# Performance work log

Hardware: AMD Instinct MI355X
Metric: run time of the kernel (lower is better)

The kernel has to match this reference:

```python
import jax, jax.numpy as jnp
import numpy as np

V, D, NL, NC = 16, 256, 4, 2
MAXL, NSTATE, DCONV, EXPAND, HEADDIM = 1024, 64, 4, 2, 64
DIN = EXPAND * D            # 512 inner channels
H = DIN // HEADDIM          # 8 heads
P = HEADDIM                 # 64 head dim
CONV_DIM = DIN + 2 * NSTATE # 640 channels through depthwise conv
D_IN_PROJ = 2 * DIN + 2 * NSTATE + H  # 1160
B_, L_ = 2, 1024
EPS = 1e-5


def setup_inputs() -> dict:
    key = jax.random.key(0)
    ks = iter(jax.random.split(key, 32))

    def rn(shape, s=0.02):
        return jax.random.normal(next(ks), shape, jnp.float32) * s

    emb = rn((V, D)).at[4].set(0.0)  # padding_idx=4 row zeroed
    pos_emb = rn((MAXL, D))
    in_proj_w = rn((NL, D_IN_PROJ, D))
    conv_w = rn((NL, CONV_DIM, DCONV), 0.1)
    conv_b = rn((NL, CONV_DIM), 0.1)
    dt_bias = rn((NL, H), 0.5)
    A_log = jnp.log(jax.random.uniform(next(ks), (NL, H), jnp.float32, 1.0, 16.0))
    D_param = jnp.ones((NL, H), jnp.float32)
    norm_w = jnp.ones((NL, DIN), jnp.float32)
    out_proj_w = rn((NL, D, DIN))
    pooler_w = rn((D, D), 0.05)
    pooler_b = jnp.zeros((D,), jnp.float32)
    cls1_w = rn((D // 2, D), 0.05)
    cls1_b = jnp.zeros((D // 2,), jnp.float32)
    cls2_w = rn((NC, D // 2), 0.05)
    cls2_b = jnp.zeros((NC,), jnp.float32)
    input_ids = jax.random.randint(next(ks), (B_, L_), 0, V)
    return dict(input_ids=input_ids, emb=emb, pos_emb=pos_emb,
                in_proj_w=in_proj_w, conv_w=conv_w, conv_b=conv_b,
                dt_bias=dt_bias, A_log=A_log, D_param=D_param, norm_w=norm_w,
                out_proj_w=out_proj_w, pooler_w=pooler_w, pooler_b=pooler_b,
                cls1_w=cls1_w, cls1_b=cls1_b, cls2_w=cls2_w, cls2_b=cls2_b)


def _mamba2(x, Win, cw, cb, dtb, A_log, Dp, nw, Wout):
    Bsz, L, _ = x.shape
    zxbcdt = jnp.einsum('bld,pd->blp', x, Win)              # (B,L,2*DIN+2N+H)
    z = zxbcdt[..., :DIN]
    xBC = zxbcdt[..., DIN:DIN + CONV_DIM]
    dt = jax.nn.softplus(zxbcdt[..., -H:] + dtb)            # (B,L,H)
    # causal depthwise conv over time
    xBC = jnp.transpose(xBC, (0, 2, 1))                     # (B,C,L)
    xBC = jax.lax.conv_general_dilated(
        xBC, cw[:, None, :], (1,), [(DCONV - 1, 0)],
        dimension_numbers=('NCH', 'OIH', 'NCH'),
        feature_group_count=CONV_DIM)
    xBC = jax.nn.silu(jnp.transpose(xBC, (0, 2, 1)) + cb)   # (B,L,C)
    xs = xBC[..., :DIN].reshape(Bsz, L, H, P)
    Bm = xBC[..., DIN:DIN + NSTATE]                         # (B,L,N)
    Cm = xBC[..., DIN + NSTATE:]                            # (B,L,N)
    A = -jnp.exp(A_log)                                     # (H,)
    dA = jnp.exp(dt * A)                                    # (B,L,H)
    dBx = dt[..., None, None] * xs[..., None] * Bm[:, :, None, None, :]  # (B,L,H,P,N)

    def step(h, inp):
        dA_t, dBx_t, C_t = inp
        h = dA_t[:, :, None, None] * h + dBx_t              # (B,H,P,N)
        y = jnp.einsum('bhpn,bn->bhp', h, C_t)
        return h, y

    h0 = jnp.zeros((Bsz, H, P, NSTATE), x.dtype)
    _, y = jax.lax.scan(step, h0, (jnp.moveaxis(dA, 1, 0),
                                   jnp.moveaxis(dBx, 1, 0),
                                   jnp.moveaxis(Cm, 1, 0)))
    y = jnp.moveaxis(y, 0, 1) + Dp[None, None, :, None] * xs  # (B,L,H,P)
    y = y.reshape(Bsz, L, DIN) * jax.nn.silu(z)               # gated
    y = y * jax.lax.rsqrt(jnp.mean(y * y, axis=-1, keepdims=True) + EPS) * nw
    return jnp.einsum('bld,od->blo', y, Wout)


def reference(input_ids, emb, pos_emb, in_proj_w, conv_w, conv_b, dt_bias,
              A_log, D_param, norm_w, out_proj_w, pooler_w, pooler_b,
              cls1_w, cls1_b, cls2_w, cls2_b):
    L = input_ids.shape[1]
    x = emb[input_ids] + pos_emb[:L][None]                  # (B,L,D)
    for i in range(NL):
        x = x + _mamba2(x, in_proj_w[i], conv_w[i], conv_b[i], dt_bias[i],
                        A_log[i], D_param[i], norm_w[i], out_proj_w[i])
    pooled = (x.mean(axis=1) + x.max(axis=1)) * 0.5         # (B,D)
    pooled = jax.nn.gelu(pooled @ pooler_w.T + pooler_b, approximate=False)
    hcls = jax.nn.gelu(pooled @ cls1_w.T + cls1_b, approximate=False)
    return hcls @ cls2_w.T + cls2_b
```

## Files before the change

### kernel.cpp

```cpp
#include <hip/hip_runtime.h>
#include <math.h>

#define D_ 256
#define NL_ 4
#define NC_ 2
#define L_LEN 1024
#define NSTATE_ 64
#define DIN_ 512
#define H_ 8
#define P_ 64
#define CONVDIM_ 640
#define DPROJ_ 1160
#define EPS_ 1e-5f
#define NCH_ 16

typedef __attribute__((ext_vector_type(8))) short short8;
typedef __attribute__((ext_vector_type(4))) float f32x4;
typedef __attribute__((ext_vector_type(4))) unsigned short us4;

__device__ __forceinline__ float siluf(float x) { return x / (1.f + __expf(-x)); }
__device__ __forceinline__ float geluf(float x) { return 0.5f * x * (1.f + erff(x * 0.70710678118654752f)); }
__device__ __forceinline__ unsigned short f2bf(float f) {
    unsigned u = __float_as_uint(f);
    u += 0x7FFFu + ((u >> 16) & 1u);
    return (unsigned short)(u >> 16);
}
__device__ __forceinline__ float bf2f(unsigned short h) {
    return __uint_as_float(((unsigned)h) << 16);
}

__global__ void k_embed(const int* __restrict__ ids, const float* __restrict__ emb,
                        const float* __restrict__ pos, float* __restrict__ x, int total) {
    int i = blockIdx.x * blockDim.x + threadIdx.x;
    if (i >= total) return;
    int d = i & (D_ - 1);
    int bl = i >> 8;
    int l = bl & (L_LEN - 1);
    x[i] = emb[ids[bl] * D_ + d] + pos[l * D_ + d];
}

__global__ void k_w2bf2(const float* __restrict__ Wi, const float* __restrict__ Wo,
                        unsigned short* __restrict__ wih, unsigned short* __restrict__ wil,
                        unsigned short* __restrict__ woh, unsigned short* __restrict__ wol,
                        int nin, int ntot) {
    int i = blockIdx.x * blockDim.x + threadIdx.x;
    if (i >= ntot) return;
    if (i < nin) {
        float f = Wi[i];
        unsigned short h = f2bf(f);
        wih[i] = h;
        wil[i] = f2bf(f - bf2f(h));
    } else {
        int j = i - nin;
        float f = Wo[j];
        unsigned short h = f2bf(f);
        woh[j] = h;
        wol[j] = f2bf(f - bf2f(h));
    }
}

__global__ void __launch_bounds__(256) gemm_bf3(const float* __restrict__ A,
        const unsigned short* __restrict__ Bhi, const unsigned short* __restrict__ Blo,
        float* __restrict__ C, int M, int N, int K, int kchunk) {
    __shared__ __align__(16) unsigned short Ah[128 * 40];
    __shared__ __align__(16) unsigned short Al[128 * 40];
    __shared__ __align__(16) unsigned short Bh[64 * 40];
    __shared__ __align__(16) unsigned short Bl[64 * 40];
    const int tid = threadIdx.x;
    const int col0 = blockIdx.x * 64;
    const int row0 = blockIdx.y * 128;
    const int kbase = blockIdx.z * kchunk;

    const int sar = tid >> 1, sas = (tid & 1) * 16;
    const int sbr = tid >> 2, sbs = (tid & 3) * 8;
    const bool bok = (col0 + sbr) < N;
    const float* aptr = A + (size_t)(row0 + sar) * K + kbase + sas;
    const unsigned short* bhptr = Bhi + (size_t)(col0 + sbr) * K + kbase + sbs;
    const unsigned short* blptr = Blo + (size_t)(col0 + sbr) * K + kbase + sbs;

    float4 pa[4];
    short8 pbh = {0, 0, 0, 0, 0, 0, 0, 0}, pbl = {0, 0, 0, 0, 0, 0, 0, 0};
#pragma unroll
    for (int i = 0; i < 4; ++i) pa[i] = *(const float4*)(aptr + i * 4);
    if (bok) {
        pbh = *(const short8*)bhptr;
        pbl = *(const short8*)blptr;
    }

    const int wave = tid >> 6, lane = tid & 63;
    const int lq = lane >> 4, lm = lane & 15;
    f32x4 acc[2][4] = {};
    const int nsteps = kchunk >> 5;
    for (int s = 0; s < nsteps; ++s) {
        __syncthreads();
#pragma unroll
        for (int i = 0; i < 4; ++i) {
            float4 f = pa[i];
            unsigned short h0 = f2bf(f.x), h1 = f2bf(f.y), h2 = f2bf(f.z), h3 = f2bf(f.w);
            us4 hv = {h0, h1, h2, h3};
            us4 lv = {f2bf(f.x - bf2f(h0)), f2bf(f.y - bf2f(h1)),
                      f2bf(f.z - bf2f(h2)), f2bf(f.w - bf2f(h3))};
            *(us4*)&Ah[sar * 40 + sas + i * 4] = hv;
            *(us4*)&Al[sar * 40 + sas + i * 4] = lv;
        }
        *(short8*)&Bh[sbr * 40 + sbs] = pbh;
        *(short8*)&Bl[sbr * 40 + sbs] = pbl;
        __syncthreads();
        if (s + 1 < nsteps) {
            int ko = (s + 1) * 32;
#pragma unroll
            for (int i = 0; i < 4; ++i) pa[i] = *(const float4*)(aptr + ko + i * 4);
            if (bok) {
                pbh = *(const short8*)(bhptr + ko);
                pbl = *(const short8*)(blptr + ko);
            }
        }
        short8 bh[4], bl[4];
#pragma unroll
        for (int ct = 0; ct < 4; ++ct) {
            bh[ct] = *(const short8*)&Bh[(ct * 16 + lm) * 40 + lq * 8];
            bl[ct] = *(const short8*)&Bl[(ct * 16 + lm) * 40 + lq * 8];
        }
#pragma unroll
        for (int rt = 0; rt < 2; ++rt) {
            short8 ah = *(const short8*)&Ah[(wave * 32 + rt * 16 + lm) * 40 + lq * 8];
            short8 al = *(const short8*)&Al[(wave * 32 + rt * 16 + lm) * 40 + lq * 8];
#pragma unroll
            for (int ct = 0; ct < 4; ++ct) {
                acc[rt][ct] = __builtin_amdgcn_mfma_f32_16x16x32_bf16(ah, bh[ct], acc[rt][ct], 0, 0, 0);
                acc[rt][ct] = __builtin_amdgcn_mfma_f32_16x16x32_bf16(ah, bl[ct], acc[rt][ct], 0, 0, 0);
                acc[rt][ct] = __builtin_amdgcn_mfma_f32_16x16x32_bf16(al, bh[ct], acc[rt][ct], 0, 0, 0);
            }
        }
    }
#pragma unroll
    for (int rt = 0; rt < 2; ++rt) {
#pragma unroll
        for (int ct = 0; ct < 4; ++ct) {
            int col = col0 + ct * 16 + lm;
            if (col >= N) continue;
            int rbase = row0 + wave * 32 + rt * 16 + lq * 4;
#pragma unroll
            for (int reg = 0; reg < 4; ++reg) {
                size_t idx = (size_t)(rbase + reg) * N + col;
                C[idx] = acc[rt][ct][reg];
            }
        }
    }
}

__global__ void __launch_bounds__(256) gemm_outs(const float* __restrict__ y,
        const float* __restrict__ nw, const float* __restrict__ rowssq,
        const unsigned short* __restrict__ Bhi, const unsigned short* __restrict__ Blo,
        float* __restrict__ x) {
    __shared__ __align__(16) unsigned short Ah[128 * 40];
    __shared__ __align__(16) unsigned short Al[128 * 40];
    __shared__ __align__(16) unsigned short Bh[64 * 40];
    __shared__ __align__(16) unsigned short Bl[64 * 40];
    const int tid = threadIdx.x;
    const int col0 = blockIdx.x * 64;
    const int row0 = blockIdx.y * 128;
    const int kbase = blockIdx.z * 128;
    const int sar = tid >> 1, sas = (tid & 1) * 16;
    const int sbr = tid >> 2, sbs = (tid & 3) * 8;
    const float* yp = y + (size_t)(row0 + sar) * DIN_ + kbase + sas;
    const unsigned short* bhptr = Bhi + (size_t)(col0 + sbr) * DIN_ + kbase + sbs;
    const unsigned short* blptr = Blo + (size_t)(col0 + sbr) * DIN_ + kbase + sbs;
    const float sc = rsqrtf(rowssq[row0 + sar] * (1.f / DIN_) + EPS_);

    float4 py[4], pnw[4];
    short8 pbh, pbl;
#pragma unroll
    for (int i = 0; i < 4; ++i) {
        py[i] = *(const float4*)(yp + i * 4);
        pnw[i] = *(const float4*)&nw[kbase + sas + i * 4];
    }
    pbh = *(const short8*)bhptr;
    pbl = *(const short8*)blptr;

    const int wave = tid >> 6, lane = tid & 63;
    const int lq = lane >> 4, lm = lane & 15;
    f32x4 acc[2][4] = {};
    for (int s = 0; s < 4; ++s) {
        __syncthreads();
#pragma unroll
        for (int i = 0; i < 4; ++i) {
            float4 fy = py[i], fn = pnw[i];
            float g0 = fy.x * sc * fn.x;
            float g1 = fy.y * sc * fn.y;
            float g2 = fy.z * sc * fn.z;
            float g3 = fy.w * sc * fn.w;
            unsigned short h0 = f2bf(g0), h1 = f2bf(g1), h2 = f2bf(g2), h3 = f2bf(g3);
            us4 hv = {h0, h1, h2, h3};
            us4 lv = {f2bf(g0 - bf2f(h0)), f2bf(g1 - bf2f(h1)),
                      f2bf(g2 - bf2f(h2)), f2bf(g3 - bf2f(h3))};
            *(us4*)&Ah[sar * 40 + sas + i * 4] = hv;
            *(us4*)&Al[sar * 40 + sas + i * 4] = lv;
        }
        *(short8*)&Bh[sbr * 40 + sbs] = pbh;
        *(short8*)&Bl[sbr * 40 + sbs] = pbl;
        __syncthreads();
        if (s + 1 < 4) {
            int ko = (s + 1) * 32;
#pragma unroll
            for (int i = 0; i < 4; ++i) {
                py[i] = *(const float4*)(yp + ko + i * 4);
                pnw[i] = *(const float4*)&nw[kbase + ko + sas + i * 4];
            }
            pbh = *(const short8*)(bhptr + ko);
            pbl = *(const short8*)(blptr + ko);
        }
        short8 bh[4], bl[4];
#pragma unroll
        for (int ct = 0; ct < 4; ++ct) {
            bh[ct] = *(const short8*)&Bh[(ct * 16 + lm) * 40 + lq * 8];
            bl[ct] = *(const short8*)&Bl[(ct * 16 + lm) * 40 + lq * 8];
        }
#pragma unroll
        for (int rt = 0; rt < 2; ++rt) {
            short8 ah = *(const short8*)&Ah[(wave * 32 + rt * 16 + lm) * 40 + lq * 8];
            short8 al = *(const short8*)&Al[(wave * 32 + rt * 16 + lm) * 40 + lq * 8];
#pragma unroll
            for (int ct = 0; ct < 4; ++ct) {
                acc[rt][ct] = __builtin_amdgcn_mfma_f32_16x16x32_bf16(ah, bh[ct], acc[rt][ct], 0, 0, 0);
                acc[rt][ct] = __builtin_amdgcn_mfma_f32_16x16x32_bf16(ah, bl[ct], acc[rt][ct], 0, 0, 0);
                acc[rt][ct] = __builtin_amdgcn_mfma_f32_16x16x32_bf16(al, bh[ct], acc[rt][ct], 0, 0, 0);
            }
        }
    }
#pragma unroll
    for (int rt = 0; rt < 2; ++rt) {
#pragma unroll
        for (int ct = 0; ct < 4; ++ct) {
            int col = col0 + ct * 16 + lm;
            int rbase = row0 + wave * 32 + rt * 16 + lq * 4;
#pragma unroll
            for (int reg = 0; reg < 4; ++reg) {
                atomicAdd(&x[(size_t)(rbase + reg) * D_ + col], acc[rt][ct][reg]);
            }
        }
    }
}

__global__ void __launch_bounds__(256) k_ssmA(const float* __restrict__ zx,
        const float* __restrict__ cw, const float* __restrict__ cb,
        const float* __restrict__ dtbias, const float* __restrict__ Alog,
        const float* __restrict__ Dp,
        float* __restrict__ Sbuf, float* __restrict__ decay,
        float* __restrict__ Ctil, float* __restrict__ y, float* __restrict__ rowssq) {
    __shared__ float U[64][65];
    __shared__ float V[64][65];
    __shared__ float W[64][65];
    __shared__ float sdt[64], cs[64], wj[64];
    const int c = blockIdx.x, bh = blockIdx.y;
    const int b = bh >> 3, h = bh & 7;
    const int l0 = c << 6;
    const int tid = threadIdx.x, wid = tid >> 6, lane = tid & 63;

    if (h == 0 && tid < 64) rowssq[b * L_LEN + l0 + tid] = 0.f;

    const int chx = h * P_ + lane;
    const int chb = DIN_ + lane;
    const int chc = DIN_ + NSTATE_ + lane;
    float wx0 = cw[chx * 4], wx1 = cw[chx * 4 + 1], wx2 = cw[chx * 4 + 2], wx3 = cw[chx * 4 + 3];
    float wb0 = cw[chb * 4], wb1 = cw[chb * 4 + 1], wb2 = cw[chb * 4 + 2], wb3 = cw[chb * 4 + 3];
    float wc0 = cw[chc * 4], wc1 = cw[chc * 4 + 1], wc2 = cw[chc * 4 + 2], wc3 = cw[chc * 4 + 3];
    float bx = cb[chx], bb = cb[chb], bc = cb[chc];

    for (int r = 0; r < 64; r += 4) {
        int j = r + wid;
        int l = l0 + j;
        float ax = bx, ab = bb, ac = bc;
#pragma unroll
        for (int k = 0; k < 4; ++k) {
            int t = l - 3 + k;
            if (t >= 0) {
                const float* row = zx + (size_t)(b * L_LEN + t) * DPROJ_;
                float wxk = (k == 0) ? wx0 : (k == 1) ? wx1 : (k == 2) ? wx2 : wx3;
                float wbk = (k == 0) ? wb0 : (k == 1) ? wb1 : (k == 2) ? wb2 : wb3;
                float wck = (k == 0) ? wc0 : (k == 1) ? wc1 : (k == 2) ? wc2 : wc3;
                ax += wxk * row[DIN_ + chx];
                ab += wbk * row[DIN_ + chb];
                ac += wck * row[DIN_ + chc];
            }
        }
        U[j][lane] = siluf(ax);
        V[j][lane] = siluf(ab);
        W[j][lane] = siluf(ac);
    }
    if (tid < 64) {
        float xv = zx[(size_t)(b * L_LEN + l0 + tid) * DPROJ_ + (DPROJ_ - H_) + h] + dtbias[h];
        float sp = fmaxf(xv, 0.f) + log1pf(__expf(-fabsf(xv)));
        sdt[tid] = sp;
        cs[tid] = sp * (-__expf(Alog[h]));
    }
    __syncthreads();
    if (tid == 0) {
        float s = 0.f;
        for (int j = 0; j < 64; ++j) { s += cs[j]; cs[j] = s; }
    }
    __syncthreads();
    if (tid < 64) wj[tid] = __expf(cs[63] - cs[tid]) * sdt[tid];
    if (tid == 0) decay[bh * NCH_ + c] = __expf(cs[63]);
    __syncthreads();

    const int t4 = (tid & 15) * 4;
    const int r4 = (tid >> 4) * 4;
    const size_t sbase = (size_t)(bh * NCH_ + c) * 4096;

    {
        float acc[4][4] = {};
        for (int j = 0; j < 64; ++j) {
            float w = wj[j];
            float4 xv = *(const float4*)&U[j][r4];
            float4 bv = *(const float4*)&V[j][t4];
            float xw[4] = {xv.x * w, xv.y * w, xv.z * w, xv.w * w};
#pragma unroll
            for (int ii = 0; ii < 4; ++ii) {
                acc[ii][0] += xw[ii] * bv.x;
                acc[ii][1] += xw[ii] * bv.y;
                acc[ii][2] += xw[ii] * bv.z;
                acc[ii][3] += xw[ii] * bv.w;
            }
        }
#pragma unroll
        for (int ii = 0; ii < 4; ++ii) {
            float4 v = {acc[ii][0], acc[ii][1], acc[ii][2], acc[ii][3]};
            *(float4*)&Sbuf[sbase + (size_t)(r4 + ii) * 64 + t4] = v;
        }
    }
    for (int r = 0; r < 64; r += 4) {
        int ii = r + wid;
        Ctil[sbase + ii * 64 + lane] = __expf(cs[ii]) * W[ii][lane];
    }
    float g[4][4] = {};
    for (int ng = 0; ng < 64; ng += 4) {
        float4 cf[4], bf[4];
#pragma unroll
        for (int ii = 0; ii < 4; ++ii) cf[ii] = *(const float4*)&W[r4 + ii][ng];
#pragma unroll
        for (int jj = 0; jj < 4; ++jj) bf[jj] = *(const float4*)&V[t4 + jj][ng];
#pragma unroll
        for (int ii = 0; ii < 4; ++ii)
#pragma unroll
            for (int jj = 0; jj < 4; ++jj)
                g[ii][jj] += cf[ii].x * bf[jj].x + cf[ii].y * bf[jj].y +
                             cf[ii].z * bf[jj].z + cf[ii].w * bf[jj].w;
    }
    float wt[4][4];
#pragma unroll
    for (int ii = 0; ii < 4; ++ii) {
        int i = r4 + ii;
        float csi = cs[i];
#pragma unroll
        for (int jj = 0; jj < 4; ++jj) {
            int j = t4 + jj;
            wt[ii][jj] = (j <= i) ? __expf(fminf(csi - cs[j], 0.f)) * sdt[j] * g[ii][jj] : 0.f;
        }
    }
    __syncthreads();
#pragma unroll
    for (int jj = 0; jj < 4; ++jj) {
        float4 v = {wt[0][jj], wt[1][jj], wt[2][jj], wt[3][jj]};
        *(float4*)&V[t4 + jj][r4] = v;
    }
    __syncthreads();
    {
        float acc[4][4] = {};
        for (int j = 0; j < 64; ++j) {
            float4 wv = *(const float4*)&V[j][r4];
            float4 xv = *(const float4*)&U[j][t4];
            float ws[4] = {wv.x, wv.y, wv.z, wv.w};
#pragma unroll
            for (int ii = 0; ii < 4; ++ii) {
                acc[ii][0] += ws[ii] * xv.x;
                acc[ii][1] += ws[ii] * xv.y;
                acc[ii][2] += ws[ii] * xv.z;
                acc[ii][3] += ws[ii] * xv.w;
            }
        }
        float Dh = Dp[h];
#pragma unroll
        for (int ii = 0; ii < 4; ++ii) {
            float4 xv = *(const float4*)&U[r4 + ii][t4];
            float4 v = {acc[ii][0] + Dh * xv.x, acc[ii][1] + Dh * xv.y,
                        acc[ii][2] + Dh * xv.z, acc[ii][3] + Dh * xv.w};
            *(float4*)&y[(size_t)(b * L_LEN + l0 + r4 + ii) * DIN_ + h * P_ + t4] = v;
        }
    }
}

__global__ void __launch_bounds__(256) k_inter(const float* __restrict__ Sbuf,
        const float* __restrict__ Ctil, const float* __restrict__ decay,
        const float* __restrict__ zx, float* __restrict__ y,
        float* __restrict__ rowssq) {
    __shared__ float Sm[64][65];
    __shared__ float Cm[64][65];
    const int c = blockIdx.x, bh = blockIdx.y;
    const int b = bh >> 3, h = bh & 7;
    const int l0 = c << 6;
    const int tid = threadIdx.x, wid = tid >> 6, lane = tid & 63;
    const size_t bhbase = (size_t)bh * NCH_ * 4096;

    float dec[NCH_];
#pragma unroll
    for (int k = 0; k < NCH_; ++k) dec[k] = decay[bh * NCH_ + k];

    float acc16[16] = {};
    float wgt = 1.f;
    for (int cp = c - 1; cp >= 0; --cp) {
        const float* src = Sbuf + bhbase + (size_t)cp * 4096;
#pragma unroll
        for (int i = 0; i < 16; ++i) acc16[i] += wgt * src[i * 256 + tid];
        wgt *= dec[cp];
    }
#pragma unroll
    for (int i = 0; i < 16; ++i) Sm[i * 4 + wid][lane] = acc16[i];

    const size_t base = bhbase + (size_t)c * 4096;
    for (int r = 0; r < 64; r += 4) {
        int pp = r + wid;
        Cm[pp][lane] = Ctil[base + pp * 64 + lane];
    }
    __syncthreads();
    const int t4 = (tid & 15) * 4;
    const int r4 = (tid >> 4) * 4;
    float acc[4][4] = {};
    if (c > 0) {
        for (int ng = 0; ng < 64; ng += 4) {
            float4 cf[4], sf[4];
#pragma unroll
            for (int ii = 0; ii < 4; ++ii) cf[ii] = *(const float4*)&Cm[r4 + ii][ng];
#pragma unroll
            for (int pp = 0; pp < 4; ++pp) sf[pp] = *(const float4*)&Sm[t4 + pp][ng];
#pragma unroll
            for (int ii = 0; ii < 4; ++ii)
#pragma unroll
                for (int pp = 0; pp < 4; ++pp)
                    acc[ii][pp] += cf[ii].x * sf[pp].x + cf[ii].y * sf[pp].y +
                                   cf[ii].z * sf[pp].z + cf[ii].w * sf[pp].w;
        }
    }
    float ssq[4];
#pragma unroll
    for (int ii = 0; ii < 4; ++ii) {
        int row = b * L_LEN + l0 + r4 + ii;
        float* dst = &y[(size_t)row * DIN_ + h * P_ + t4];
        const float* zr = &zx[(size_t)row * DPROJ_ + h * P_ + t4];
        float4 v = *(const float4*)dst;
        float4 z = *(const float4*)zr;
        v.x = (v.x + acc[ii][0]) * siluf(z.x);
        v.y = (v.y + acc[ii][1]) * siluf(z.y);
        v.z = (v.z + acc[ii][2]) * siluf(z.z);
        v.w = (v.w + acc[ii][3]) * siluf(z.w);
        *(float4*)dst = v;
        ssq[ii] = v.x * v.x + v.y * v.y + v.z * v.z + v.w * v.w;
    }
#pragma unroll
    for (int o = 1; o < 16; o <<= 1) {
#pragma unroll
        for (int ii = 0; ii < 4; ++ii) ssq[ii] += __shfl_xor(ssq[ii], o, 64);
    }
    if ((tid & 15) == 0) {
#pragma unroll
        for (int ii = 0; ii < 4; ++ii)
            atomicAdd(&rowssq[b * L_LEN + l0 + r4 + ii], ssq[ii]);
    }
}

__global__ void k_poolhead(const float* __restrict__ x,
                           const float* __restrict__ pw, const float* __restrict__ pb,
                           const float* __restrict__ c1w, const float* __restrict__ c1b,
                           const float* __restrict__ c2w, const float* __restrict__ c2b,
                           float* __restrict__ out) {
    __shared__ float sp[256], s1[256], s2[128];
    int b = blockIdx.x, t = threadIdx.x;
    const float* xb = x + (size_t)b * L_LEN * D_ + t;
    float a0 = 0.f, a1 = 0.f, a2 = 0.f, a3 = 0.f, m = -INFINITY;
    for (int l = 0; l < L_LEN; l += 4) {
        float v0 = xb[(size_t)l * D_];
        float v1 = xb[(size_t)(l + 1) * D_];
        float v2 = xb[(size_t)(l + 2) * D_];
        float v3 = xb[(size_t)(l + 3) * D_];
        a0 += v0; a1 += v1; a2 += v2; a3 += v3;
        m = fmaxf(m, fmaxf(fmaxf(v0, v1), fmaxf(v2, v3)));
    }
    sp[t] = ((a0 + a1 + a2 + a3) * (1.f / L_LEN) + m) * 0.5f;
    __syncthreads();
    float acc = pb[t];
    for (int d = 0; d < 256; ++d) acc += sp[d] * pw[t * 256 + d];
    s1[t] = geluf(acc);
    __syncthreads();
    if (t < 128) {
        float a = c1b[t];
        for (int d = 0; d < 256; ++d) a += s1[d] * c1w[t * 256 + d];
        s2[t] = geluf(a);
    }
    __syncthreads();
    if (t < 2) {
        float a = c2b[t];
        for (int d = 0; d < 128; ++d) a += s2[d] * c2w[t * 128 + d];
        out[b * NC_ + t] = a;
    }
}

extern "C" void kernel_launch(void* const* d_in, const int* in_sizes, int n_in,
                              void* d_out, int out_size, void* d_ws, size_t ws_size,
                              hipStream_t stream) {
    const int* ids    = (const int*)d_in[0];
    const float* emb  = (const float*)d_in[1];
    const float* pos  = (const float*)d_in[2];
    const float* Wins = (const float*)d_in[3];
    const float* cw   = (const float*)d_in[4];
    const float* cb   = (const float*)d_in[5];
    const float* dtb  = (const float*)d_in[6];
    const float* Alog = (const float*)d_in[7];
    const float* Dpar = (const float*)d_in[8];
    const float* nw   = (const float*)d_in[9];
    const float* Wout = (const float*)d_in[10];
    const float* pw   = (const float*)d_in[11];
    const float* pb   = (const float*)d_in[12];
    const float* c1w  = (const float*)d_in[13];
    const float* c1b  = (const float*)d_in[14];
    const float* c2w  = (const float*)d_in[15];
    const float* c2b  = (const float*)d_in[16];
    float* out = (float*)d_out;

    const int NWIN = NL_ * DPROJ_ * D_;
    const int NWOUT = NL_ * D_ * DIN_;

    float* ws = (float*)d_ws;
    float* x      = ws;
    float* zx     = x + 524288;
    float* y      = zx + 2375680;
    float* Sbuf   = y + 1048576;
    float* Ctil   = Sbuf + 1048576;
    float* decay  = Ctil + 1048576;
    float* rowssq = decay + 256;
    unsigned short* winh = (unsigned short*)(rowssq + 2048);
    unsigned short* winl = winh + NWIN;
    unsigned short* woh  = winl + NWIN;
    unsigned short* wol  = woh + NWOUT;

    k_w2bf2<<<(NWIN + NWOUT + 255) / 256, 256, 0, stream>>>(
        Wins, Wout, winh, winl, woh, wol, NWIN, NWIN + NWOUT);
    k_embed<<<2048, 256, 0, stream>>>(ids, emb, pos, x, 524288);
    for (int i = 0; i < NL_; ++i) {
        size_t wo_in = (size_t)i * DPROJ_ * D_;
        size_t wo_out = (size_t)i * D_ * DIN_;
        gemm_bf3<<<dim3(19, 16, 1), 256, 0, stream>>>(
            x, winh + wo_in, winl + wo_in, zx, 2048, DPROJ_, D_, D_);
        k_ssmA<<<dim3(NCH_, 16), 256, 0, stream>>>(
            zx, cw + (size_t)i * CONVDIM_ * 4, cb + (size_t)i * CONVDIM_,
            dtb + i * H_, Alog + i * H_, Dpar + i * H_, Sbuf, decay, Ctil, y, rowssq);
        k_inter<<<dim3(NCH_, 16), 256, 0, stream>>>(Sbuf, Ctil, decay, zx, y, rowssq);
        gemm_outs<<<dim3(4, 16, 4), 256, 0, stream>>>(
            y, nw + (size_t)i * DIN_, rowssq, woh + wo_out, wol + wo_out, x);
    }
    k_poolhead<<<2, 256, 0, stream>>>(x, pw, pb, c1w, c1b, c2w, c2b, out);
}
```

Before: 419.0 us.

## Precompute bf16 hi/lo splits of GEMM activations and fold norm weight into Wout

```diff
diff --git a/kernel.cpp b/kernel.cpp
--- a/kernel.cpp
+++ b/kernel.cpp
@@ -30,16 +30,33 @@
 }
 
 __global__ void k_embed(const int* __restrict__ ids, const float* __restrict__ emb,
-                        const float* __restrict__ pos, float* __restrict__ x, int total) {
+                        const float* __restrict__ pos, float* __restrict__ x,
+                        unsigned short* __restrict__ xh, unsigned short* __restrict__ xl,
+                        int total) {
     int i = blockIdx.x * blockDim.x + threadIdx.x;
     if (i >= total) return;
     int d = i & (D_ - 1);
     int bl = i >> 8;
     int l = bl & (L_LEN - 1);
-    x[i] = emb[ids[bl] * D_ + d] + pos[l * D_ + d];
+    float f = emb[ids[bl] * D_ + d] + pos[l * D_ + d];
+    x[i] = f;
+    unsigned short h = f2bf(f);
+    xh[i] = h;
+    xl[i] = f2bf(f - bf2f(h));
+}
+
+__global__ void k_x2bf(const float* __restrict__ x, unsigned short* __restrict__ xh,
+                       unsigned short* __restrict__ xl, int n) {
+    int i = blockIdx.x * blockDim.x + threadIdx.x;
+    if (i >= n) return;
+    float f = x[i];
+    unsigned short h = f2bf(f);
+    xh[i] = h;
+    xl[i] = f2bf(f - bf2f(h));
 }
 
 __global__ void k_w2bf2(const float* __restrict__ Wi, const float* __restrict__ Wo,
+                        const float* __restrict__ nw,
                         unsigned short* __restrict__ wih, unsigned short* __restrict__ wil,
                         unsigned short* __restrict__ woh, unsigned short* __restrict__ wol,
                         int nin, int ntot) {
@@ -52,16 +69,19 @@
         wil[i] = f2bf(f - bf2f(h));
     } else {
         int j = i - nin;
-        float f = Wo[j];
+        int layer = j / (D_ * DIN_);
+        int k = j % DIN_;
+        float f = Wo[j] * nw[layer * DIN_ + k];
         unsigned short h = f2bf(f);
         woh[j] = h;
         wol[j] = f2bf(f - bf2f(h));
     }
 }
 
-__global__ void __launch_bounds__(256) gemm_bf3(const float* __restrict__ A,
+__global__ void __launch_bounds__(256) gemm_bf3b(const unsigned short* __restrict__ Ahg,
+        const unsigned short* __restrict__ Alg,
         const unsigned short* __restrict__ Bhi, const unsigned short* __restrict__ Blo,
-        float* __restrict__ C, int M, int N, int K, int kchunk) {
+        float* __restrict__ C, int M, int N, int K) {
     __shared__ __align__(16) unsigned short Ah[128 * 40];
     __shared__ __align__(16) unsigned short Al[128 * 40];
     __shared__ __align__(16) unsigned short Bh[64 * 40];
@@ -69,19 +89,18 @@
     const int tid = threadIdx.x;
     const int col0 = blockIdx.x * 64;
     const int row0 = blockIdx.y * 128;
-    const int kbase = blockIdx.z * kchunk;
 
     const int sar = tid >> 1, sas = (tid & 1) * 16;
     const int sbr = tid >> 2, sbs = (tid & 3) * 8;
     const bool bok = (col0 + sbr) < N;
-    const float* aptr = A + (size_t)(row0 + sar) * K + kbase + sas;
-    const unsigned short* bhptr = Bhi + (size_t)(col0 + sbr) * K + kbase + sbs;
-    const unsigned short* blptr = Blo + (size_t)(col0 + sbr) * K + kbase + sbs;
-
-    float4 pa[4];
+    const unsigned short* ahptr = Ahg + (size_t)(row0 + sar) * K + sas;
+    const unsigned short* alptr = Alg + (size_t)(row0 + sar) * K + sas;
+    const unsigned short* bhptr = Bhi + (size_t)(col0 + sbr) * K + sbs;
+    const unsigned short* blptr = Blo + (size_t)(col0 + sbr) * K + sbs;
+
+    short8 pah0 = *(const short8*)ahptr, pah1 = *(const short8*)(ahptr + 8);
+    short8 pal0 = *(const short8*)alptr, pal1 = *(const short8*)(alptr + 8);
     short8 pbh = {0, 0, 0, 0, 0, 0, 0, 0}, pbl = {0, 0, 0, 0, 0, 0, 0, 0};
-#pragma unroll
-    for (int i = 0; i < 4; ++i) pa[i] = *(const float4*)(aptr + i * 4);
     if (bok) {
         pbh = *(const short8*)bhptr;
         pbl = *(const short8*)blptr;
@@ -90,26 +109,22 @@
     const int wave = tid >> 6, lane = tid & 63;
     const int lq = lane >> 4, lm = lane & 15;
     f32x4 acc[2][4] = {};
-    const int nsteps = kchunk >> 5;
+    const int nsteps = K >> 5;
     for (int s = 0; s < nsteps; ++s) {
         __syncthreads();
-#pragma unroll
-        for (int i = 0; i < 4; ++i) {
-            float4 f = pa[i];
-            unsigned short h0 = f2bf(f.x), h1 = f2bf(f.y), h2 = f2bf(f.z), h3 = f2bf(f.w);
-            us4 hv = {h0, h1, h2, h3};
-            us4 lv = {f2bf(f.x - bf2f(h0)), f2bf(f.y - bf2f(h1)),
-                      f2bf(f.z - bf2f(h2)), f2bf(f.w - bf2f(h3))};
-            *(us4*)&Ah[sar * 40 + sas + i * 4] = hv;
-            *(us4*)&Al[sar * 40 + sas + i * 4] = lv;
-        }
+        *(short8*)&Ah[sar * 40 + sas] = pah0;
+        *(short8*)&Ah[sar * 40 + sas + 8] = pah1;
+        *(short8*)&Al[sar * 40 + sas] = pal0;
+        *(short8*)&Al[sar * 40 + sas + 8] = pal1;
         *(short8*)&Bh[sbr * 40 + sbs] = pbh;
         *(short8*)&Bl[sbr * 40 + sbs] = pbl;
         __syncthreads();
         if (s + 1 < nsteps) {
             int ko = (s + 1) * 32;
-#pragma unroll
-            for (int i = 0; i < 4; ++i) pa[i] = *(const float4*)(aptr + ko + i * 4);
+            pah0 = *(const short8*)(ahptr + ko);
+            pah1 = *(const short8*)(ahptr + ko + 8);
+            pal0 = *(const short8*)(alptr + ko);
+            pal1 = *(const short8*)(alptr + ko + 8);
             if (bok) {
                 pbh = *(const short8*)(bhptr + ko);
                 pbl = *(const short8*)(blptr + ko);
@@ -142,15 +157,14 @@
             int rbase = row0 + wave * 32 + rt * 16 + lq * 4;
 #pragma unroll
             for (int reg = 0; reg < 4; ++reg) {
-                size_t idx = (size_t)(rbase + reg) * N + col;
-                C[idx] = acc[rt][ct][reg];
-            }
-        }
-    }
-}
-
-__global__ void __launch_bounds__(256) gemm_outs(const float* __restrict__ y,
-        const float* __restrict__ nw, const float* __restrict__ rowssq,
+                C[(size_t)(rbase + reg) * N + col] = acc[rt][ct][reg];
+            }
+        }
+    }
+}
+
+__global__ void __launch_bounds__(256) gemm_outs(const unsigned short* __restrict__ Ghg,
+        const unsigned short* __restrict__ Glg, const float* __restrict__ rowssq,
         const unsigned short* __restrict__ Bhi, const unsigned short* __restrict__ Blo,
         float* __restrict__ x) {
     __shared__ __align__(16) unsigned short Ah[128 * 40];
@@ -163,50 +177,33 @@
     const int kbase = blockIdx.z * 128;
     const int sar = tid >> 1, sas = (tid & 1) * 16;
     const int sbr = tid >> 2, sbs = (tid & 3) * 8;
-    const float* yp = y + (size_t)(row0 + sar) * DIN_ + kbase + sas;
+    const unsigned short* ahptr = Ghg + (size_t)(row0 + sar) * DIN_ + kbase + sas;
+    const unsigned short* alptr = Glg + (size_t)(row0 + sar) * DIN_ + kbase + sas;
     const unsigned short* bhptr = Bhi + (size_t)(col0 + sbr) * DIN_ + kbase + sbs;
     const unsigned short* blptr = Blo + (size_t)(col0 + sbr) * DIN_ + kbase + sbs;
-    const float sc = rsqrtf(rowssq[row0 + sar] * (1.f / DIN_) + EPS_);
-
-    float4 py[4], pnw[4];
-    short8 pbh, pbl;
-#pragma unroll
-    for (int i = 0; i < 4; ++i) {
-        py[i] = *(const float4*)(yp + i * 4);
-        pnw[i] = *(const float4*)&nw[kbase + sas + i * 4];
-    }
-    pbh = *(const short8*)bhptr;
-    pbl = *(const short8*)blptr;
+
+    short8 pah0 = *(const short8*)ahptr, pah1 = *(const short8*)(ahptr + 8);
+    short8 pal0 = *(const short8*)alptr, pal1 = *(const short8*)(alptr + 8);
+    short8 pbh = *(const short8*)bhptr, pbl = *(const short8*)blptr;
 
     const int wave = tid >> 6, lane = tid & 63;
     const int lq = lane >> 4, lm = lane & 15;
     f32x4 acc[2][4] = {};
     for (int s = 0; s < 4; ++s) {
         __syncthreads();
-#pragma unroll
-        for (int i = 0; i < 4; ++i) {
-            float4 fy = py[i], fn = pnw[i];
-            float g0 = fy.x * sc * fn.x;
-            float g1 = fy.y * sc * fn.y;
-            float g2 = fy.z * sc * fn.z;
-            float g3 = fy.w * sc * fn.w;
-            unsigned short h0 = f2bf(g0), h1 = f2bf(g1), h2 = f2bf(g2), h3 = f2bf(g3);
-            us4 hv = {h0, h1, h2, h3};
-            us4 lv = {f2bf(g0 - bf2f(h0)), f2bf(g1 - bf2f(h1)),
-                      f2bf(g2 - bf2f(h2)), f2bf(g3 - bf2f(h3))};
-            *(us4*)&Ah[sar * 40 + sas + i * 4] = hv;
-            *(us4*)&Al[sar * 40 + sas + i * 4] = lv;
-        }
+        *(short8*)&Ah[sar * 40 + sas] = pah0;
+        *(short8*)&Ah[sar * 40 + sas + 8] = pah1;
+        *(short8*)&Al[sar * 40 + sas] = pal0;
+        *(short8*)&Al[sar * 40 + sas + 8] = pal1;
         *(short8*)&Bh[sbr * 40 + sbs] = pbh;
         *(short8*)&Bl[sbr * 40 + sbs] = pbl;
         __syncthreads();
         if (s + 1 < 4) {
             int ko = (s + 1) * 32;
-#pragma unroll
-            for (int i = 0; i < 4; ++i) {
-                py[i] = *(const float4*)(yp + ko + i * 4);
-                pnw[i] = *(const float4*)&nw[kbase + ko + sas + i * 4];
-            }
+            pah0 = *(const short8*)(ahptr + ko);
+            pah1 = *(const short8*)(ahptr + ko + 8);
+            pal0 = *(const short8*)(alptr + ko);
+            pal1 = *(const short8*)(alptr + ko + 8);
             pbh = *(const short8*)(bhptr + ko);
             pbl = *(const short8*)(blptr + ko);
         }
@@ -230,13 +227,17 @@
     }
 #pragma unroll
     for (int rt = 0; rt < 2; ++rt) {
+        int rbase = row0 + wave * 32 + rt * 16 + lq * 4;
+        float sc[4];
+#pragma unroll
+        for (int reg = 0; reg < 4; ++reg)
+            sc[reg] = rsqrtf(rowssq[rbase + reg] * (1.f / DIN_) + EPS_);
 #pragma unroll
         for (int ct = 0; ct < 4; ++ct) {
             int col = col0 + ct * 16 + lm;
-            int rbase = row0 + wave * 32 + rt * 16 + lq * 4;
 #pragma unroll
             for (int reg = 0; reg < 4; ++reg) {
-                atomicAdd(&x[(size_t)(rbase + reg) * D_ + col], acc[rt][ct][reg]);
+                atomicAdd(&x[(size_t)(rbase + reg) * D_ + col], sc[reg] * acc[rt][ct][reg]);
             }
         }
     }
@@ -392,7 +393,8 @@
 
 __global__ void __launch_bounds__(256) k_inter(const float* __restrict__ Sbuf,
         const float* __restrict__ Ctil, const float* __restrict__ decay,
-        const float* __restrict__ zx, float* __restrict__ y,
+        const float* __restrict__ zx, const float* __restrict__ y,
+        unsigned short* __restrict__ gh, unsigned short* __restrict__ gl,
         float* __restrict__ rowssq) {
     __shared__ float Sm[64][65];
     __shared__ float Cm[64][65];
@@ -445,15 +447,20 @@
 #pragma unroll
     for (int ii = 0; ii < 4; ++ii) {
         int row = b * L_LEN + l0 + r4 + ii;
-        float* dst = &y[(size_t)row * DIN_ + h * P_ + t4];
+        const float* yr = &y[(size_t)row * DIN_ + h * P_ + t4];
         const float* zr = &zx[(size_t)row * DPROJ_ + h * P_ + t4];
-        float4 v = *(const float4*)dst;
+        float4 v = *(const float4*)yr;
         float4 z = *(const float4*)zr;
         v.x = (v.x + acc[ii][0]) * siluf(z.x);
         v.y = (v.y + acc[ii][1]) * siluf(z.y);
         v.z = (v.z + acc[ii][2]) * siluf(z.z);
         v.w = (v.w + acc[ii][3]) * siluf(z.w);
-        *(float4*)dst = v;
+        unsigned short h0 = f2bf(v.x), h1 = f2bf(v.y), h2 = f2bf(v.z), h3 = f2bf(v.w);
+        us4 hv = {h0, h1, h2, h3};
+        us4 lv = {f2bf(v.x - bf2f(h0)), f2bf(v.y - bf2f(h1)),
+                  f2bf(v.z - bf2f(h2)), f2bf(v.w - bf2f(h3))};
+        *(us4*)&gh[(size_t)row * DIN_ + h * P_ + t4] = hv;
+        *(us4*)&gl[(size_t)row * DIN_ + h * P_ + t4] = lv;
         ssq[ii] = v.x * v.x + v.y * v.y + v.z * v.z + v.w * v.w;
     }
 #pragma unroll
@@ -468,39 +475,50 @@
     }
 }
 
-__global__ void k_poolhead(const float* __restrict__ x,
+__global__ void __launch_bounds__(1024) k_poolhead(const float* __restrict__ x,
                            const float* __restrict__ pw, const float* __restrict__ pb,
                            const float* __restrict__ c1w, const float* __restrict__ c1b,
                            const float* __restrict__ c2w, const float* __restrict__ c2b,
                            float* __restrict__ out) {
+    __shared__ float ps[4][256], pm[4][256];
     __shared__ float sp[256], s1[256], s2[128];
-    int b = blockIdx.x, t = threadIdx.x;
-    const float* xb = x + (size_t)b * L_LEN * D_ + t;
-    float a0 = 0.f, a1 = 0.f, a2 = 0.f, a3 = 0.f, m = -INFINITY;
-    for (int l = 0; l < L_LEN; l += 4) {
+    int b = blockIdx.x, tid = threadIdx.x;
+    int t = tid & 255, grp = tid >> 8;
+    const float* xb = x + (size_t)b * L_LEN * D_ + (size_t)grp * 256 * D_ + t;
+    float s = 0.f, m = -INFINITY;
+    for (int l = 0; l < 256; l += 4) {
         float v0 = xb[(size_t)l * D_];
         float v1 = xb[(size_t)(l + 1) * D_];
         float v2 = xb[(size_t)(l + 2) * D_];
         float v3 = xb[(size_t)(l + 3) * D_];
-        a0 += v0; a1 += v1; a2 += v2; a3 += v3;
+        s += v0 + v1 + v2 + v3;
         m = fmaxf(m, fmaxf(fmaxf(v0, v1), fmaxf(v2, v3)));
     }
-    sp[t] = ((a0 + a1 + a2 + a3) * (1.f / L_LEN) + m) * 0.5f;
-    __syncthreads();
-    float acc = pb[t];
-    for (int d = 0; d < 256; ++d) acc += sp[d] * pw[t * 256 + d];
-    s1[t] = geluf(acc);
-    __syncthreads();
-    if (t < 128) {
-        float a = c1b[t];
-        for (int d = 0; d < 256; ++d) a += s1[d] * c1w[t * 256 + d];
-        s2[t] = geluf(a);
-    }
-    __syncthreads();
-    if (t < 2) {
-        float a = c2b[t];
-        for (int d = 0; d < 128; ++d) a += s2[d] * c2w[t * 128 + d];
-        out[b * NC_ + t] = a;
+    ps[grp][t] = s;
+    pm[grp][t] = m;
+    __syncthreads();
+    if (grp == 0) {
+        float ss = ps[0][t] + ps[1][t] + ps[2][t] + ps[3][t];
+        float mm = fmaxf(fmaxf(pm[0][t], pm[1][t]), fmaxf(pm[2][t], pm[3][t]));
+        sp[t] = (ss * (1.f / L_LEN) + mm) * 0.5f;
+    }
+    __syncthreads();
+    if (tid < 256) {
+        float acc = pb[tid];
+        for (int d = 0; d < 256; ++d) acc += sp[d] * pw[tid * 256 + d];
+        s1[tid] = geluf(acc);
+    }
+    __syncthreads();
+    if (tid < 128) {
+        float a = c1b[tid];
+        for (int d = 0; d < 256; ++d) a += s1[d] * c1w[tid * 256 + d];
+        s2[tid] = geluf(a);
+    }
+    __syncthreads();
+    if (tid < 2) {
+        float a = c2b[tid];
+        for (int d = 0; d < 128; ++d) a += s2[d] * c2w[tid * 128 + d];
+        out[b * NC_ + tid] = a;
     }
 }
 
@@ -528,6 +546,8 @@
 
     const int NWIN = NL_ * DPROJ_ * D_;
     const int NWOUT = NL_ * D_ * DIN_;
+    const int NX = 524288;
+    const int NG = 1048576;
 
     float* ws = (float*)d_ws;
     float* x      = ws;
@@ -541,21 +561,27 @@
     unsigned short* winl = winh + NWIN;
     unsigned short* woh  = winl + NWIN;
     unsigned short* wol  = woh + NWOUT;
+    unsigned short* xh   = wol + NWOUT;
+    unsigned short* xl   = xh + NX;
+    unsigned short* gh   = xl + NX;
+    unsigned short* gl   = gh + NG;
 
     k_w2bf2<<<(NWIN + NWOUT + 255) / 256, 256, 0, stream>>>(
-        Wins, Wout, winh, winl, woh, wol, NWIN, NWIN + NWOUT);
-    k_embed<<<2048, 256, 0, stream>>>(ids, emb, pos, x, 524288);
+        Wins, Wout, nw, winh, winl, woh, wol, NWIN, NWIN + NWOUT);
+    k_embed<<<2048, 256, 0, stream>>>(ids, emb, pos, x, xh, xl, NX);
     for (int i = 0; i < NL_; ++i) {
         size_t wo_in = (size_t)i * DPROJ_ * D_;
         size_t wo_out = (size_t)i * D_ * DIN_;
-        gemm_bf3<<<dim3(19, 16, 1), 256, 0, stream>>>(
-            x, winh + wo_in, winl + wo_in, zx, 2048, DPROJ_, D_, D_);
+        gemm_bf3b<<<dim3(19, 16), 256, 0, stream>>>(
+            xh, xl, winh + wo_in, winl + wo_in, zx, 2048, DPROJ_, D_);
         k_ssmA<<<dim3(NCH_, 16), 256, 0, stream>>>(
             zx, cw + (size_t)i * CONVDIM_ * 4, cb + (size_t)i * CONVDIM_,
             dtb + i * H_, Alog + i * H_, Dpar + i * H_, Sbuf, decay, Ctil, y, rowssq);
-        k_inter<<<dim3(NCH_, 16), 256, 0, stream>>>(Sbuf, Ctil, decay, zx, y, rowssq);
+        k_inter<<<dim3(NCH_, 16), 256, 0, stream>>>(Sbuf, Ctil, decay, zx, y, gh, gl, rowssq);
         gemm_outs<<<dim3(4, 16, 4), 256, 0, stream>>>(
-            y, nw + (size_t)i * DIN_, rowssq, woh + wo_out, wol + wo_out, x);
-    }
-    k_poolhead<<<2, 256, 0, stream>>>(x, pw, pb, c1w, c1b, c2w, c2b, out);
-}
+            gh, gl, rowssq, woh + wo_out, wol + wo_out, x);
+        if (i < NL_ - 1)
+            k_x2bf<<<2048, 256, 0, stream>>>(x, xh, xl, NX);
+    }
+    k_poolhead<<<2, 1024, 0, stream>>>(x, pw, pb, c1w, c1b, c2w, c2b, out);
+}
```

Result: no change. 414.4 us (-1.1%).
